# Performance work log

Hardware: AMD Instinct MI355X
Metric: run time of the kernel (lower is better)

## Reference

```python
import jax, jax.numpy as jnp
import numpy as np

DIM = 128
NUM_HEADS = 2
HEAD_DIM = DIM // NUM_HEADS
SCALE = HEAD_DIM ** -0.5
SR = 4
EPS_LN = 1e-5


def token2map(x, idx_token, H, W, H_init, W_init):
    """Scatter tokens x[B,N,Cc] into a [B,Cc,H,W] map via the init grid.
    Matches the sparse-COO branch of the torch token2map (N_init < N*H*W).
    """
    B, N, Cc = x.shape
    N_init = H_init * W_init
    # nearest-neighbor index of each init-grid cell in the HxW map
    rows = (jnp.arange(H_init) * H) // H_init          # floor(i * H / H_init)
    cols = (jnp.arange(W_init) * W) // W_init
    idx_hw = (rows[:, None] * W + cols[None, :]).reshape(-1)      # [N_init]
    flat = (idx_hw[None, :] + jnp.arange(B)[:, None] * (H * W)).reshape(-1)  # [B*N_init]
    # per-pixel count (A @ ones) + 1e-6, as in torch
    count = jax.ops.segment_sum(jnp.ones((B * N_init,), jnp.float32), flat,
                                num_segments=B * H * W) + 1e-6    # [B*H*W]
    gathered = jnp.take_along_axis(x, idx_token[..., None], axis=1)  # [B,N_init,Cc]
    out = jax.ops.segment_sum(gathered.reshape(B * N_init, Cc), flat,
                              num_segments=B * H * W)
    out = out / count[:, None]
    return out.reshape(B, H, W, Cc).transpose(0, 3, 1, 2)  # [B,Cc,H,W]


def setup_inputs() -> dict:
    key = jax.random.key(0)
    ks = jax.random.split(key, 12)
    B, Nq, Nkv, C = 8, 12544, 12544, DIM
    H, W, H_init, W_init = 112, 112, 224, 224
    inp = {
        'q_x': jax.random.normal(ks[0], (B, Nq, C), jnp.float32),
        'kv_x': jax.random.normal(ks[1], (B, Nkv, C), jnp.float32),
        'token_score': jax.random.normal(ks[2], (B, Nkv, 1), jnp.float32),
        'idx_token': jax.random.randint(ks[3], (B, H_init * W_init), 0, Nkv),
        'H': H, 'W': W, 'H_init': H_init, 'W_init': W_init,
        # learned params (qkv_bias=False)
        'q_w': jax.random.normal(ks[4], (C, C), jnp.float32) * 0.02,
        'kv_w': jax.random.normal(ks[5], (C, 2 * C), jnp.float32) * 0.02,
        'proj_w': jax.random.normal(ks[6], (C, C), jnp.float32) * 0.02,
        'proj_b': jnp.zeros((C,), jnp.float32),
        'sr_w': jax.random.normal(ks[7], (C, C, SR, SR), jnp.float32) * np.sqrt(2.0 / (SR * SR * C)),
        'sr_b': jnp.zeros((C,), jnp.float32),
        'norm_g': jnp.ones((C,), jnp.float32),
        'norm_b': jnp.zeros((C,), jnp.float32),
    }
    return inp


def reference(q_x, kv_x, token_score, q_w, kv_w, proj_w, proj_b, sr_w, sr_b,
              norm_g, norm_b, idx_token, H, W, H_init, W_init):
    B, Nq, C = q_x.shape
    # q projection -> [B, h, Nq, d]
    q = (q_x @ q_w).reshape(B, Nq, NUM_HEADS, HEAD_DIM).transpose(0, 2, 1, 3)

    # sr_ratio > 1 path: scatter kv tokens (with conf channel) to q's map
    tmp = jnp.concatenate([kv_x, token_score], axis=-1)          # [B,Nkv,C+1]
    tmp_map = token2map(tmp, idx_token, H, W, H_init, W_init)    # [B,C+1,H,W]
    kv_map = tmp_map[:, :C]                                      # [B,C,H,W]
    conf_map = tmp_map[:, C:]                                    # [B,1,H,W]

    # spatial reduction conv (kernel=stride=SR) + LayerNorm
    kv_r = jax.lax.conv_general_dilated(
        kv_map, sr_w, window_strides=(SR, SR), padding='VALID',
        dimension_numbers=('NCHW', 'OIHW', 'NCHW')) + sr_b[None, :, None, None]
    h, w = kv_r.shape[2], kv_r.shape[3]
    Ns = h * w
    kv_t = kv_r.reshape(B, C, Ns).transpose(0, 2, 1)             # [B,Ns,C]
    mu = jnp.mean(kv_t, axis=-1, keepdims=True)
    var = jnp.mean(jnp.square(kv_t - mu), axis=-1, keepdims=True)
    kv_t = (kv_t - mu) / jnp.sqrt(var + EPS_LN) * norm_g + norm_b

    # avg-pool conf to the reduced grid
    conf = conf_map.reshape(B, 1, h, SR, w, SR).mean(axis=(3, 5)).reshape(B, Ns)

    # kv projection -> k,v [B,h,Ns,d]
    kv_p = (kv_t @ kv_w).reshape(B, Ns, 2, NUM_HEADS, HEAD_DIM).transpose(2, 0, 3, 1, 4)
    k, v = kv_p[0], kv_p[1]

    attn = jnp.einsum('bhqd,bhkd->bhqk', q * SCALE, k) + conf[:, None, None, :]
    attn = jax.nn.softmax(attn, axis=-1)
    out = jnp.einsum('bhqk,bhkd->bhqd', attn, v).transpose(0, 2, 1, 3).reshape(B, Nq, C)
    return out @ proj_w + proj_b
```

## Files before the change

### kernel.cpp

```cpp
#include <hip/hip_runtime.h>
#include <hip/hip_bf16.h>


#define NBATCH 8
#define NQTOK  12544
#define NSP    832
#define LOG2E  1.4426950408889634f
#define QSCALE (0.125f * LOG2E)

typedef __attribute__((ext_vector_type(8))) short bf8;
typedef __attribute__((ext_vector_type(4))) float f4;
typedef __attribute__((ext_vector_type(4))) unsigned short u16x4;
typedef __attribute__((ext_vector_type(2))) unsigned int u32x2;

#define MFMA16(a, b, c) __builtin_amdgcn_mfma_f32_16x16x32_bf16((a), (b), (c), 0, 0, 0)

#if __has_builtin(__builtin_amdgcn_exp2f)
#define EXP2(x) __builtin_amdgcn_exp2f(x)
#else
#define EXP2(x) exp2f(x)
#endif

__device__ __forceinline__ unsigned short f2b(float x) {
  union { float f; unsigned u; } v; v.f = x;
  unsigned r = v.u + 0x7FFFu + ((v.u >> 16) & 1u);
  return (unsigned short)(r >> 16);
}

__device__ __forceinline__ unsigned pk2(float lo, float hi) {
  float2 t; t.x = lo; t.y = hi;
  __hip_bfloat162 bb = __float22bfloat162_rn(t);
  union { __hip_bfloat162 b; unsigned u; } v; v.b = bb;
  return v.u;
}

__device__ __forceinline__ bf8 rows2frag(const unsigned W0[2], const unsigned W1[2]) {
  u32x2 r0 = __builtin_amdgcn_permlane32_swap(W0[0], W1[0], false, false);
  u32x2 t02 = __builtin_amdgcn_permlane16_swap(r0.x, r0.y, false, false);
  u32x2 r1 = __builtin_amdgcn_permlane32_swap(W0[1], W1[1], false, false);
  u32x2 t13 = __builtin_amdgcn_permlane16_swap(r1.x, r1.y, false, false);
  union { unsigned u[4]; bf8 v; } pa;
  pa.u[0] = t02.x; pa.u[1] = t13.x; pa.u[2] = t02.y; pa.u[3] = t13.y;
  return pa.v;
}

__device__ __forceinline__ bf8 ldfrag(const unsigned short* t, int stride, int rbase, int kbase) {
  int lane = threadIdx.x & 63;
  return *(const bf8*)(t + (rbase + (lane & 15)) * stride + kbase + ((lane >> 4) << 3));
}

__global__ void k_setup(const float* __restrict__ qw, const float* __restrict__ kvw,
                        const float* __restrict__ pw, const float* __restrict__ srw,
                        unsigned short* __restrict__ qwt, unsigned short* __restrict__ kvwt,
                        unsigned short* __restrict__ pwt, unsigned short* __restrict__ srwt,
                        unsigned* __restrict__ kb, unsigned* __restrict__ vb,
                        float* __restrict__ conf) {
  int tid = blockIdx.x * 256 + threadIdx.x;
  int nt = gridDim.x * 256;
  for (int i = tid; i < 128 * 128; i += nt) {
    int k = i >> 7, n = i & 127;
    qwt[n * 128 + k] = f2b(qw[k * 128 + n] * QSCALE);
    pwt[n * 128 + k] = f2b(pw[k * 128 + n]);
  }
  for (int i = tid; i < 128 * 256; i += nt) {
    int k = i >> 8, j = i & 255;
    kvwt[j * 128 + k] = f2b(kvw[k * 256 + j]);
  }
  for (int i = tid; i < 128 * 2048; i += nt) {
    int o = i >> 11, kk = i & 2047;
    int p = kk >> 7, c = kk & 127;
    srwt[o * 2048 + kk] = f2b(srw[o * 2048 + c * 16 + p]);
  }
  const int nu = NBATCH * 2 * NSP * 64 / 2;
  for (int i = tid; i < nu; i += nt) { kb[i] = 0u; vb[i] = 0u; }
  for (int i = tid; i < NBATCH * NSP; i += nt) conf[i] = -1e30f;
}

__global__ void k_token2map(const float* __restrict__ kv_x, const float* __restrict__ tsc,
                            const int* __restrict__ idxt,
                            unsigned short* __restrict__ kv_map, float* __restrict__ conf_map) {
  int tid = threadIdx.x;
  int bid = blockIdx.x;
  int b = bid & 7, pos = bid >> 3;
  int hw = pos * 8 + (tid >> 5);
  int cell = b * 12544 + hw;
  int c0 = (tid & 31) << 2;
  int h = hw / 112, w = hw - h * 112;
  const int* it = idxt + b * 50176;
  int t0 = it[(2 * h) * 224 + 2 * w];
  int t1 = it[(2 * h) * 224 + 2 * w + 1];
  int t2 = it[(2 * h + 1) * 224 + 2 * w];
  int t3 = it[(2 * h + 1) * 224 + 2 * w + 1];
  const float* base = kv_x + (long)b * 12544 * 128 + c0;
  const float recip = 1.0f / (4.0f + 1e-6f);
  float4 a0 = *(const float4*)(base + (long)t0 * 128);
  float4 a1 = *(const float4*)(base + (long)t1 * 128);
  float4 a2 = *(const float4*)(base + (long)t2 * 128);
  float4 a3 = *(const float4*)(base + (long)t3 * 128);
  u16x4 o;
  o[0] = f2b((a0.x + a1.x + a2.x + a3.x) * recip);
  o[1] = f2b((a0.y + a1.y + a2.y + a3.y) * recip);
  o[2] = f2b((a0.z + a1.z + a2.z + a3.z) * recip);
  o[3] = f2b((a0.w + a1.w + a2.w + a3.w) * recip);
  *(u16x4*)(kv_map + (long)cell * 128 + c0) = o;
  if ((tid & 31) == 0) {
    const float* ts = tsc + b * 12544;
    conf_map[cell] = (ts[t0] + ts[t1] + ts[t2] + ts[t3]) * recip;
  }
}

__launch_bounds__(256)
__global__ void k_conv_ln_kv(const unsigned short* __restrict__ kv_map,
                             const unsigned short* __restrict__ srwt,
                             const float* __restrict__ srb, const float* __restrict__ ng,
                             const float* __restrict__ nb,
                             const unsigned short* __restrict__ kvwt,
                             unsigned short* __restrict__ kbuf,
                             unsigned short* __restrict__ vbuf,
                             const float* __restrict__ conf_map, float* __restrict__ conf) {
  __shared__ unsigned short At[64 * 136];
  __shared__ unsigned short Bt[128 * 136];
  const int tid = threadIdx.x;
  const int lane = tid & 63, w = tid >> 6;
  const int l15 = lane & 15, g = lane >> 4;
  const int r0 = blockIdx.x * 64;
  if (tid < 64) {
    int pos = r0 + tid;
    int bq = pos / 784, p2 = pos - bq * 784;
    int oh = p2 / 28, ow = p2 - oh * 28;
    float s = 0.f;
#pragma unroll
    for (int kh = 0; kh < 4; kh++)
#pragma unroll
      for (int kw = 0; kw < 4; kw++)
        s += conf_map[bq * 12544 + (4 * oh + kh) * 112 + 4 * ow + kw];
    conf[bq * NSP + p2] = s * (LOG2E / 16.0f);
  }
  const f4 fz = {0.f, 0.f, 0.f, 0.f};
  f4 acc[8];
#pragma unroll
  for (int i = 0; i < 8; i++) acc[i] = fz;

  for (int p = 0; p < 16; p++) {
#pragma unroll
    for (int j = 0; j < 4; j++) {
      int id = tid + 256 * j;
      int row = id >> 4, c0 = (id & 15) << 3;
      int rr = r0 + row;
      int bb = rr / 784, pos = rr - bb * 784;
      int oh = pos / 28, ow = pos - oh * 28;
      long src = ((long)(bb * 12544 + (4 * oh + (p >> 2)) * 112 + 4 * ow + (p & 3))) * 128 + c0;
      *(uint4*)(At + row * 136 + c0) = *(const uint4*)(kv_map + src);
    }
#pragma unroll
    for (int j = 0; j < 8; j++) {
      int id = tid + 256 * j;
      int row = id >> 4, c0 = (id & 15) << 3;
      *(uint4*)(Bt + row * 136 + c0) = *(const uint4*)(srwt + row * 2048 + p * 128 + c0);
    }
    __syncthreads();
#pragma unroll
    for (int ks = 0; ks < 4; ks++) {
      bf8 a = ldfrag(At, 136, 16 * w, 32 * ks);
#pragma unroll
      for (int nf = 0; nf < 8; nf++) {
        bf8 bb = ldfrag(Bt, 136, 16 * nf, 32 * ks);
        acc[nf] = MFMA16(a, bb, acc[nf]);
      }
    }
    __syncthreads();
  }
  float sum_[4] = {0.f, 0.f, 0.f, 0.f}, sq_[4] = {0.f, 0.f, 0.f, 0.f};
#pragma unroll
  for (int nf = 0; nf < 8; nf++) {
    float bias = srb[16 * nf + l15];
#pragma unroll
    for (int reg = 0; reg < 4; reg++) {
      float v = acc[nf][reg] + bias;
      acc[nf][reg] = v;
      sum_[reg] += v;
      sq_[reg] += v * v;
    }
  }
#pragma unroll
  for (int msk = 1; msk < 16; msk <<= 1)
#pragma unroll
    for (int reg = 0; reg < 4; reg++) {
      sum_[reg] += __shfl_xor(sum_[reg], msk, 64);
      sq_[reg] += __shfl_xor(sq_[reg], msk, 64);
    }
#pragma unroll
  for (int nf = 0; nf < 8; nf++) {
    float gc = ng[16 * nf + l15], bc = nb[16 * nf + l15];
#pragma unroll
    for (int reg = 0; reg < 4; reg++) {
      float mean = sum_[reg] * (1.0f / 128.0f);
      float var = sq_[reg] * (1.0f / 128.0f) - mean * mean;
      float v = (acc[nf][reg] - mean) * rsqrtf(var + 1e-5f) * gc + bc;
      At[(16 * w + 4 * g + reg) * 136 + 16 * nf + l15] = f2b(v);
    }
  }
  __syncthreads();
  f4 acc2[16];
#pragma unroll
  for (int i = 0; i < 16; i++) acc2[i] = fz;
#pragma unroll
  for (int ks = 0; ks < 4; ks++) {
    bf8 a = ldfrag(At, 136, 16 * w, 32 * ks);
#pragma unroll
    for (int nf = 0; nf < 16; nf++) {
      bf8 bb = *(const bf8*)(kvwt + (16 * nf + l15) * 128 + 32 * ks + (g << 3));
      acc2[nf] = MFMA16(a, bb, acc2[nf]);
    }
  }
#pragma unroll
  for (int nf = 0; nf < 16; nf++)
#pragma unroll
    for (int reg = 0; reg < 4; reg++) {
      int r = r0 + 16 * w + 4 * g + reg;
      int b = r / 784, ns = r - b * 784;
      int j = 16 * nf + l15;
      int sel = j >> 7, hh = (j >> 6) & 1, d = j & 63;
      unsigned short val = f2b(acc2[nf][reg]);
      if (sel == 0) kbuf[((long)(b * 2 + hh) * NSP + ns) * 64 + d] = val;
      else          vbuf[((long)(b * 2 + hh) * 64 + d) * NSP + ns] = val;
    }
}

__launch_bounds__(256)
__global__ void k_q(const float* __restrict__ q_x, const unsigned short* __restrict__ qwt,
                    unsigned short* __restrict__ qbuf) {
  __shared__ unsigned short At[64 * 136];
  __shared__ unsigned short Bt[128 * 136];
  const int tid = threadIdx.x;
  const int lane = tid & 63, w = tid >> 6;
  const int l15 = lane & 15, g = lane >> 4;
  const int r0 = blockIdx.x * 64;
#pragma unroll
  for (int j = 0; j < 8; j++) {
    int id = tid + 256 * j;
    int row = id >> 5, c0 = (id & 31) << 2;
    float4 v = *(const float4*)(q_x + (long)(r0 + row) * 128 + c0);
    u16x4 o;
    o[0] = f2b(v.x); o[1] = f2b(v.y); o[2] = f2b(v.z); o[3] = f2b(v.w);
    *(u16x4*)(At + row * 136 + c0) = o;
  }
#pragma unroll
  for (int j = 0; j < 8; j++) {
    int id = tid + 256 * j;
    int row = id >> 4, c0 = (id & 15) << 3;
    *(uint4*)(Bt + row * 136 + c0) = *(const uint4*)(qwt + (long)row * 128 + c0);
  }
  __syncthreads();
  const f4 fz = {0.f, 0.f, 0.f, 0.f};
  f4 acc[8];
#pragma unroll
  for (int i = 0; i < 8; i++) acc[i] = fz;
#pragma unroll
  for (int ks = 0; ks < 4; ks++) {
    bf8 a = ldfrag(At, 136, 16 * w, 32 * ks);
#pragma unroll
    for (int nf = 0; nf < 8; nf++) {
      bf8 bb = ldfrag(Bt, 136, 16 * nf, 32 * ks);
      acc[nf] = MFMA16(a, bb, acc[nf]);
    }
  }
#pragma unroll
  for (int nf = 0; nf < 8; nf++)
#pragma unroll
    for (int reg = 0; reg < 4; reg++) {
      int r = r0 + 16 * w + 4 * g + reg;
      int b = r / NQTOK, n = r - b * NQTOK;
      int j = 16 * nf + l15;
      int hh = j >> 6, d = j & 63;
      qbuf[((long)(b * 2 + hh) * NQTOK + n) * 64 + d] = f2b(acc[nf][reg]);
    }
}

__launch_bounds__(256, 3)
__global__ void k_attn(const unsigned short* __restrict__ qbuf,
                       const unsigned short* __restrict__ kbuf,
                       const unsigned short* __restrict__ vbuf,
                       const float* __restrict__ conf,
                       unsigned short* __restrict__ attbuf) {
  __shared__ unsigned short Kt[2][64 * 72];
  __shared__ unsigned short Vt[2][64 * 72];
  const int tid = threadIdx.x;
  const int lane = tid & 63, w = tid >> 6;
  const int l15 = lane & 15, g = lane >> 4;
  const int bid = blockIdx.x;
  const int xcd = bid & 7, idx = bid >> 3;
  const int sub = idx / 98;
  const int xb = idx - sub * 98;
  const int bhid = xcd * 2 + sub;
  const int b = bhid >> 1, h = bhid & 1;
  const int bh = b * 2 + h;
  const int q0 = xb * 128 + 32 * w;

  const unsigned short* qsrc = qbuf + ((long)bh * NQTOK + q0) * 64;
  bf8 qf[2][2];
#pragma unroll
  for (int mr = 0; mr < 2; mr++)
#pragma unroll
    for (int ks = 0; ks < 2; ks++)
      qf[mr][ks] = *(const bf8*)(qsrc + (16 * mr + l15) * 64 + 32 * ks + (g << 3));

  const int srow = tid >> 2;
  const int scol = (tid & 3) << 4;
  const unsigned short* kg = kbuf + (long)bh * NSP * 64 + srow * 64 + scol;
  const unsigned short* vg = vbuf + (long)bh * 64 * NSP + (long)srow * NSP + scol;
  unsigned short* klds = &Kt[0][0] + srow * 72 + scol;
  unsigned short* vlds = &Vt[0][0] + srow * 72 + scol;

  uint4 kr0, kr1, vr0, vr1;
#define ISSUE(T)                                                   \
  do {                                                             \
    const unsigned short* kp_ = kg + (long)(T) * 4096;             \
    const unsigned short* vp_ = vg + (T) * 64;                     \
    kr0 = *(const uint4*)(kp_);                                    \
    kr1 = *(const uint4*)(kp_ + 8);                                \
    vr0 = *(const uint4*)(vp_);                                    \
    vr1 = *(const uint4*)(vp_ + 8);                                \
  } while (0)
#define STWRITE(BUF)                                               \
  do {                                                             \
    unsigned short* kd_ = klds + (BUF) * 4608;                     \
    unsigned short* vd_ = vlds + (BUF) * 4608;                     \
    *(uint4*)kd_ = kr0;  *(uint4*)(kd_ + 8) = kr1;                 \
    *(uint4*)vd_ = vr0;  *(uint4*)(vd_ + 8) = vr1;                 \
  } while (0)

  ISSUE(0);
  STWRITE(0);
  ISSUE(1);
  __syncthreads();

  const f4 fz = {0.f, 0.f, 0.f, 0.f};
  f4 ao[2][4], aol[2];
#pragma unroll
  for (int mr = 0; mr < 2; mr++) {
    aol[mr] = fz;
#pragma unroll
    for (int i = 0; i < 4; i++) ao[mr][i] = fz;
  }
  const short on = (short)0x3F80;
  const bf8 onesf = {on, on, on, on, on, on, on, on};
  const float* confb = conf + b * NSP;

#pragma unroll 2
  for (int t = 0; t < 13; t++) {
    const int cur = t & 1;
    const unsigned short* KtB = &Kt[cur][0];
    const unsigned short* VtB = &Vt[cur][0];
    bf8 kf[4][2];
#pragma unroll
    for (int mf = 0; mf < 4; mf++)
#pragma unroll
      for (int ks = 0; ks < 2; ks++)
        kf[mf][ks] = ldfrag(KtB, 72, 16 * mf, 32 * ks);
    bf8 vf[4][2];
#pragma unroll
    for (int nfd = 0; nfd < 4; nfd++)
#pragma unroll
      for (int ks = 0; ks < 2; ks++)
        vf[nfd][ks] = ldfrag(VtB, 72, 16 * nfd, 32 * ks);
    float4 cv[4];
#pragma unroll
    for (int mf = 0; mf < 4; mf++)
      cv[mf] = *(const float4*)(confb + t * 64 + 16 * mf + 4 * g);
#pragma unroll
    for (int mr = 0; mr < 2; mr++) {
      f4 s_[4];
#pragma unroll
      for (int mf = 0; mf < 4; mf++) s_[mf] = fz;
#pragma unroll
      for (int ks = 0; ks < 2; ks++)
#pragma unroll
        for (int mf = 0; mf < 4; mf++)
          s_[mf] = MFMA16(kf[mf][ks], qf[mr][ks], s_[mf]);
      unsigned W[4][2];
#pragma unroll
      for (int mf = 0; mf < 4; mf++) {
        float p0 = EXP2(s_[mf][0] + cv[mf].x);
        float p1 = EXP2(s_[mf][1] + cv[mf].y);
        float p2 = EXP2(s_[mf][2] + cv[mf].z);
        float p3 = EXP2(s_[mf][3] + cv[mf].w);
        W[mf][0] = pk2(p0, p1);
        W[mf][1] = pk2(p2, p3);
      }
#pragma unroll
      for (int ks = 0; ks < 2; ks++) {
        bf8 pa = rows2frag(W[2 * ks], W[2 * ks + 1]);
        aol[mr] = MFMA16(pa, onesf, aol[mr]);
#pragma unroll
        for (int nfd = 0; nfd < 4; nfd++)
          ao[mr][nfd] = MFMA16(pa, vf[nfd][ks], ao[mr][nfd]);
      }
    }
    if (t < 12) STWRITE(cur ^ 1);
    if (t < 11) ISSUE(t + 2);
    __syncthreads();
  }
#undef ISSUE
#undef STWRITE
#pragma unroll
  for (int mr = 0; mr < 2; mr++) {
    float inv[4];
#pragma unroll
    for (int reg = 0; reg < 4; reg++) inv[reg] = 1.0f / aol[mr][reg];
#pragma unroll
    for (int nfd = 0; nfd < 4; nfd++)
#pragma unroll
      for (int reg = 0; reg < 4; reg++) {
        int n = q0 + 16 * mr + 4 * g + reg;
        int col = h * 64 + 16 * nfd + l15;
        attbuf[((long)b * NQTOK + n) * 128 + col] = f2b(ao[mr][nfd][reg] * inv[reg]);
      }
  }
}

__launch_bounds__(256)
__global__ void k_proj(const unsigned short* __restrict__ attbuf,
                       const unsigned short* __restrict__ pwt,
                       const float* __restrict__ pb, float* __restrict__ out) {
  __shared__ unsigned short At[64 * 136];
  __shared__ unsigned short Bt[128 * 136];
  const int tid = threadIdx.x;
  const int lane = tid & 63, w = tid >> 6;
  const int l15 = lane & 15, g = lane >> 4;
  const int r0 = blockIdx.x * 64;
#pragma unroll
  for (int j = 0; j < 4; j++) {
    int id = tid + 256 * j;
    int row = id >> 4, c0 = (id & 15) << 3;
    *(uint4*)(At + row * 136 + c0) = *(const uint4*)(attbuf + (long)(r0 + row) * 128 + c0);
  }
#pragma unroll
  for (int j = 0; j < 8; j++) {
    int id = tid + 256 * j;
    int row = id >> 4, c0 = (id & 15) << 3;
    *(uint4*)(Bt + row * 136 + c0) = *(const uint4*)(pwt + (long)row * 128 + c0);
  }
  __syncthreads();
  const f4 fz = {0.f, 0.f, 0.f, 0.f};
  f4 acc[8];
#pragma unroll
  for (int i = 0; i < 8; i++) acc[i] = fz;
#pragma unroll
  for (int ks = 0; ks < 4; ks++) {
    bf8 a = ldfrag(At, 136, 16 * w, 32 * ks);
#pragma unroll
    for (int nf = 0; nf < 8; nf++) {
      bf8 bb = ldfrag(Bt, 136, 16 * nf, 32 * ks);
      acc[nf] = MFMA16(a, bb, acc[nf]);
    }
  }
#pragma unroll
  for (int nf = 0; nf < 8; nf++) {
    float bias = pb[16 * nf + l15];
#pragma unroll
    for (int reg = 0; reg < 4; reg++) {
      int r = r0 + 16 * w + 4 * g + reg;
      out[(long)r * 128 + 16 * nf + l15] = acc[nf][reg] + bias;
    }
  }
}

extern "C" void kernel_launch(void* const* d_in, const int* in_sizes, int n_in,
                              void* d_out, int out_size, void* d_ws, size_t ws_size,
                              hipStream_t stream) {
  const float* q_x  = (const float*)d_in[0];
  const float* kv_x = (const float*)d_in[1];
  const float* tsc  = (const float*)d_in[2];
  const int*   idxt = (const int*)d_in[3];
  const float* q_w  = (const float*)d_in[8];
  const float* kv_w = (const float*)d_in[9];
  const float* pw   = (const float*)d_in[10];
  const float* pb   = (const float*)d_in[11];
  const float* srw  = (const float*)d_in[12];
  const float* srb  = (const float*)d_in[13];
  const float* ng   = (const float*)d_in[14];
  const float* nb   = (const float*)d_in[15];
  float* outp = (float*)d_out;

  char* ws = (char*)d_ws;
  size_t off = 0;
  auto take = [&](size_t bytes) {
    char* p = ws + off;
    off += (bytes + 255) & ~(size_t)255;
    return p;
  };
  unsigned short* qwt   = (unsigned short*)take(128 * 128 * 2);
  unsigned short* pwt   = (unsigned short*)take(128 * 128 * 2);
  unsigned short* kvwt  = (unsigned short*)take(256 * 128 * 2);
  unsigned short* srwt  = (unsigned short*)take(128 * 2048 * 2);
  unsigned short* kvmap = (unsigned short*)take((size_t)NBATCH * 12544 * 128 * 2);
  float* conf_map       = (float*)take((size_t)NBATCH * 12544 * 4);
  unsigned short* kbuf  = (unsigned short*)take((size_t)NBATCH * 2 * NSP * 64 * 2);
  unsigned short* vbuf  = (unsigned short*)take((size_t)NBATCH * 2 * NSP * 64 * 2);
  float* conf           = (float*)take((size_t)NBATCH * NSP * 4);
  unsigned short* qbuf  = (unsigned short*)take((size_t)NBATCH * 2 * NQTOK * 64 * 2);
  unsigned short* attbuf = kvmap;

  k_setup<<<512, 256, 0, stream>>>(q_w, kv_w, pw, srw, qwt, kvwt, pwt, srwt,
                                   (unsigned*)kbuf, (unsigned*)vbuf, conf);
  k_token2map<<<12544, 256, 0, stream>>>(kv_x, tsc, idxt, kvmap, conf_map);
  k_conv_ln_kv<<<98, 256, 0, stream>>>(kvmap, srwt, srb, ng, nb, kvwt, kbuf, vbuf,
                                       conf_map, conf);
  k_q<<<1568, 256, 0, stream>>>(q_x, qwt, qbuf);
  k_attn<<<1568, 256, 0, stream>>>(qbuf, kbuf, vbuf, conf, attbuf);
  k_proj<<<1568, 256, 0, stream>>>(attbuf, pwt, pb, outp);
}
```

Before: 161.0 us.

## Fold setup into token2map, seed scores with conf, raise attn occupancy, remap q/proj blocks

```diff
diff --git a/kernel.cpp b/kernel.cpp
--- a/kernel.cpp
+++ b/kernel.cpp
@@ -49,38 +49,39 @@
   return *(const bf8*)(t + (rbase + (lane & 15)) * stride + kbase + ((lane >> 4) << 3));
 }
 
-__global__ void k_setup(const float* __restrict__ qw, const float* __restrict__ kvw,
-                        const float* __restrict__ pw, const float* __restrict__ srw,
-                        unsigned short* __restrict__ qwt, unsigned short* __restrict__ kvwt,
-                        unsigned short* __restrict__ pwt, unsigned short* __restrict__ srwt,
-                        unsigned* __restrict__ kb, unsigned* __restrict__ vb,
-                        float* __restrict__ conf) {
-  int tid = blockIdx.x * 256 + threadIdx.x;
-  int nt = gridDim.x * 256;
-  for (int i = tid; i < 128 * 128; i += nt) {
-    int k = i >> 7, n = i & 127;
-    qwt[n * 128 + k] = f2b(qw[k * 128 + n] * QSCALE);
-    pwt[n * 128 + k] = f2b(pw[k * 128 + n]);
-  }
-  for (int i = tid; i < 128 * 256; i += nt) {
-    int k = i >> 8, j = i & 255;
-    kvwt[j * 128 + k] = f2b(kvw[k * 256 + j]);
-  }
-  for (int i = tid; i < 128 * 2048; i += nt) {
-    int o = i >> 11, kk = i & 2047;
-    int p = kk >> 7, c = kk & 127;
-    srwt[o * 2048 + kk] = f2b(srw[o * 2048 + c * 16 + p]);
-  }
-  const int nu = NBATCH * 2 * NSP * 64 / 2;
-  for (int i = tid; i < nu; i += nt) { kb[i] = 0u; vb[i] = 0u; }
-  for (int i = tid; i < NBATCH * NSP; i += nt) conf[i] = -1e30f;
-}
-
 __global__ void k_token2map(const float* __restrict__ kv_x, const float* __restrict__ tsc,
                             const int* __restrict__ idxt,
-                            unsigned short* __restrict__ kv_map, float* __restrict__ conf_map) {
+                            unsigned short* __restrict__ kv_map, float* __restrict__ conf_map,
+                            const float* __restrict__ qw, const float* __restrict__ kvw,
+                            const float* __restrict__ pw, const float* __restrict__ srw,
+                            unsigned short* __restrict__ qwt, unsigned short* __restrict__ kvwt,
+                            unsigned short* __restrict__ pwt, unsigned short* __restrict__ srwt,
+                            unsigned* __restrict__ kb, unsigned* __restrict__ vb,
+                            float* __restrict__ conf) {
   int tid = threadIdx.x;
   int bid = blockIdx.x;
+  if (bid >= 12544) {
+    int t = (bid - 12544) * 256 + tid;
+    int nt = 256 * 256;
+    for (int i = t; i < 128 * 128; i += nt) {
+      int k = i >> 7, n = i & 127;
+      qwt[n * 128 + k] = f2b(qw[k * 128 + n] * QSCALE);
+      pwt[n * 128 + k] = f2b(pw[k * 128 + n]);
+    }
+    for (int i = t; i < 128 * 256; i += nt) {
+      int k = i >> 8, j = i & 255;
+      kvwt[j * 128 + k] = f2b(kvw[k * 256 + j]);
+    }
+    for (int i = t; i < 128 * 2048; i += nt) {
+      int o = i >> 11, kk = i & 2047;
+      int p = kk >> 7, c = kk & 127;
+      srwt[o * 2048 + kk] = f2b(srw[o * 2048 + c * 16 + p]);
+    }
+    const int nu = NBATCH * 2 * NSP * 64 / 2;
+    for (int i = t; i < nu; i += nt) { kb[i] = 0u; vb[i] = 0u; }
+    for (int i = t; i < NBATCH * NSP; i += nt) conf[i] = -1e30f;
+    return;
+  }
   int b = bid & 7, pos = bid >> 3;
   int hw = pos * 8 + (tid >> 5);
   int cell = b * 12544 + hw;
@@ -235,7 +236,8 @@
   const int tid = threadIdx.x;
   const int lane = tid & 63, w = tid >> 6;
   const int l15 = lane & 15, g = lane >> 4;
-  const int r0 = blockIdx.x * 64;
+  const int bid = blockIdx.x;
+  const int r0 = (bid & 7) * NQTOK + (bid >> 3) * 64;
 #pragma unroll
   for (int j = 0; j < 8; j++) {
     int id = tid + 256 * j;
@@ -277,7 +279,7 @@
     }
 }
 
-__launch_bounds__(256, 3)
+__launch_bounds__(256, 4)
 __global__ void k_attn(const unsigned short* __restrict__ qbuf,
                        const unsigned short* __restrict__ kbuf,
                        const unsigned short* __restrict__ vbuf,
@@ -364,15 +366,17 @@
 #pragma unroll
       for (int ks = 0; ks < 2; ks++)
         vf[nfd][ks] = ldfrag(VtB, 72, 16 * nfd, 32 * ks);
-    float4 cv[4];
-#pragma unroll
-    for (int mf = 0; mf < 4; mf++)
-      cv[mf] = *(const float4*)(confb + t * 64 + 16 * mf + 4 * g);
+    f4 cvi[4];
+#pragma unroll
+    for (int mf = 0; mf < 4; mf++) {
+      float4 cv = *(const float4*)(confb + t * 64 + 16 * mf + 4 * g);
+      cvi[mf][0] = cv.x; cvi[mf][1] = cv.y; cvi[mf][2] = cv.z; cvi[mf][3] = cv.w;
+    }
 #pragma unroll
     for (int mr = 0; mr < 2; mr++) {
       f4 s_[4];
 #pragma unroll
-      for (int mf = 0; mf < 4; mf++) s_[mf] = fz;
+      for (int mf = 0; mf < 4; mf++) s_[mf] = cvi[mf];
 #pragma unroll
       for (int ks = 0; ks < 2; ks++)
 #pragma unroll
@@ -381,10 +385,10 @@
       unsigned W[4][2];
 #pragma unroll
       for (int mf = 0; mf < 4; mf++) {
-        float p0 = EXP2(s_[mf][0] + cv[mf].x);
-        float p1 = EXP2(s_[mf][1] + cv[mf].y);
-        float p2 = EXP2(s_[mf][2] + cv[mf].z);
-        float p3 = EXP2(s_[mf][3] + cv[mf].w);
+        float p0 = EXP2(s_[mf][0]);
+        float p1 = EXP2(s_[mf][1]);
+        float p2 = EXP2(s_[mf][2]);
+        float p3 = EXP2(s_[mf][3]);
         W[mf][0] = pk2(p0, p1);
         W[mf][1] = pk2(p2, p3);
       }
@@ -428,7 +432,8 @@
   const int tid = threadIdx.x;
   const int lane = tid & 63, w = tid >> 6;
   const int l15 = lane & 15, g = lane >> 4;
-  const int r0 = blockIdx.x * 64;
+  const int bid = blockIdx.x;
+  const int r0 = (bid & 7) * NQTOK + (bid >> 3) * 64;
 #pragma unroll
   for (int j = 0; j < 4; j++) {
     int id = tid + 256 * j;
@@ -502,9 +507,9 @@
   unsigned short* qbuf  = (unsigned short*)take((size_t)NBATCH * 2 * NQTOK * 64 * 2);
   unsigned short* attbuf = kvmap;
 
-  k_setup<<<512, 256, 0, stream>>>(q_w, kv_w, pw, srw, qwt, kvwt, pwt, srwt,
-                                   (unsigned*)kbuf, (unsigned*)vbuf, conf);
-  k_token2map<<<12544, 256, 0, stream>>>(kv_x, tsc, idxt, kvmap, conf_map);
+  k_token2map<<<12800, 256, 0, stream>>>(kv_x, tsc, idxt, kvmap, conf_map,
+                                         q_w, kv_w, pw, srw, qwt, kvwt, pwt, srwt,
+                                         (unsigned*)kbuf, (unsigned*)vbuf, conf);
   k_conv_ln_kv<<<98, 256, 0, stream>>>(kvmap, srwt, srb, ng, nb, kvwt, kbuf, vbuf,
                                        conf_map, conf);
   k_q<<<1568, 256, 0, stream>>>(q_x, qwt, qbuf);
```

Result: slower. 311.9 us (+93.8%).
